# Optimization experiments

Hardware: AMD Instinct MI355X
Metric: run time of the kernel (lower is better)

Reference implementation:

```python
import jax, jax.numpy as jnp
import numpy as np

# SoftmaxMatMulSparse forward: out = softmax(x1, dim=-1) @ x2.
# The masker/sparsify/quantize path only compresses activations saved for
# backward; the forward output is the exact dense softmax-matmul.

def setup_inputs() -> dict:
    key = jax.random.key(0)
    k1, k2 = jax.random.split(key)
    x1 = jax.random.normal(k1, (1, 16, 2048, 2048), dtype=jnp.float32)  # [B,H,S,S] scores
    x2 = jax.random.normal(k2, (1, 16, 2048, 64), dtype=jnp.float32)    # [B,H,S,Dh] values
    return {"x1": x1, "x2": x2}

def reference(x1, x2):
    probs = jax.nn.softmax(x1, axis=-1)          # [B,H,S,S]
    return jnp.matmul(probs, x2)                 # [B,H,S,Dh]
```

## Files before the change

### kernel.cpp

```cpp
#include <hip/hip_runtime.h>
#include <hip/hip_bf16.h>
#include <stdint.h>


#define H_  16
#define S_  2048
#define D_  64
#define KT  128
#define QT  64

typedef short bf16x8 __attribute__((ext_vector_type(8)));
typedef float f32x4  __attribute__((ext_vector_type(4)));

__device__ __forceinline__ uint16_t f2bf(float f) {
  uint32_t u = __builtin_bit_cast(uint32_t, f);
  u += 0x7fffu + ((u >> 16) & 1u);
  return (uint16_t)(u >> 16);
}

__global__ __launch_bounds__(256) void vtrans_kernel(const float* __restrict__ x2,
                                                     uint16_t* __restrict__ x2t) {
  __shared__ float t[D_][64 + 1];
  const int h  = blockIdx.x >> 5;
  const int k0 = (blockIdx.x & 31) << 6;
  const float* src = x2 + ((size_t)h * S_ + k0) * D_;
#pragma unroll
  for (int p = 0; p < 4; ++p) {
    int flat = p * 1024 + threadIdx.x * 4;
    int k = flat >> 6, d = flat & 63;
    float4 v = *(const float4*)(src + (size_t)k * D_ + d);
    t[d + 0][k] = v.x; t[d + 1][k] = v.y; t[d + 2][k] = v.z; t[d + 3][k] = v.w;
  }
  __syncthreads();
  uint16_t* dst = x2t + (size_t)h * D_ * S_ + k0;
#pragma unroll
  for (int p = 0; p < 4; ++p) {
    int flat = p * 1024 + threadIdx.x * 4;
    int d = flat >> 6, k = flat & 63;
    ushort4 o;
    o.x = f2bf(t[d][k + 0]); o.y = f2bf(t[d][k + 1]);
    o.z = f2bf(t[d][k + 2]); o.w = f2bf(t[d][k + 3]);
    *(ushort4*)(dst + (size_t)d * S_ + k) = o;
  }
}

__global__ __launch_bounds__(256) void smm_kernel(const float* __restrict__ x1,
                                                  const float* __restrict__ x2,
                                                  const uint16_t* __restrict__ x2t,
                                                  int use_t,
                                                  float* __restrict__ out) {
  __shared__ __attribute__((aligned(16))) uint16_t pT[QT][KT];
  __shared__ __attribute__((aligned(16))) uint16_t vT[D_][KT];

  const int tid  = threadIdx.x;
  const int lane = tid & 63;
  const int w    = tid >> 6;
  const int h    = blockIdx.x >> 5;
  const int q0   = (blockIdx.x & 31) * QT;

  f32x4 acc[4];
  f32x4 accS;
#pragma unroll
  for (int c = 0; c < 4; ++c) acc[c] = (f32x4){0.f, 0.f, 0.f, 0.f};
  accS = (f32x4){0.f, 0.f, 0.f, 0.f};

  bf16x8 ones;
  {
    short v = ((lane & 15) == 0) ? (short)0x3F80 : (short)0;
#pragma unroll
    for (int e = 0; e < 8; ++e) ones[e] = v;
  }

  const float* x1p = x1 + ((size_t)h * S_ + q0) * S_;
  const int prow = tid >> 5;
  const int pk4  = (tid & 31) << 2;
  const int arow = lane & 15;
  const int kgrp = lane >> 4;

  for (int kt = 0; kt < S_ / KT; ++kt) {
    __syncthreads();

#pragma unroll
    for (int p = 0; p < 8; ++p) {
      int r = prow + p * 8;
      float4 v = *(const float4*)(x1p + (size_t)r * S_ + kt * KT + pk4);
      uint32_t lo = (uint32_t)f2bf(__expf(v.x)) | ((uint32_t)f2bf(__expf(v.y)) << 16);
      uint32_t hi = (uint32_t)f2bf(__expf(v.z)) | ((uint32_t)f2bf(__expf(v.w)) << 16);
      int byteoff = (pk4 * 2) ^ ((r & 15) << 4);
      *(uint2*)((char*)(&pT[r][0]) + byteoff) = make_uint2(lo, hi);
    }

    if (use_t) {
      const uint16_t* vp = x2t + (size_t)h * D_ * S_ + kt * KT;
#pragma unroll
      for (int p = 0; p < 4; ++p) {
        int flat = p * 256 + tid;
        int dd = flat >> 4;
        int ch = flat & 15;
        uint4 v = *(const uint4*)(vp + (size_t)dd * S_ + ch * 8);
        int byteoff = (ch * 16) ^ ((dd & 15) << 4);
        *(uint4*)((char*)(&vT[dd][0]) + byteoff) = v;
      }
    } else {
      int dd = tid & 63;
      int kg = tid >> 6;
      const float* src = x2 + ((size_t)h * S_ + kt * KT) * D_ + dd;
#pragma unroll
      for (int p = 0; p < 4; ++p) {
        int kb = p * 32 + kg * 8;
        uint16_t tmp[8];
#pragma unroll
        for (int j = 0; j < 8; ++j) tmp[j] = f2bf(src[(size_t)(kb + j) * D_]);
        int byteoff = (kb * 2) ^ ((dd & 15) << 4);
        *(uint4*)((char*)(&vT[dd][0]) + byteoff) = *(uint4*)tmp;
      }
    }
    __syncthreads();

#pragma unroll
    for (int ks = 0; ks < 4; ++ks) {
      int kb = ks * 64 + kgrp * 16;
      int ar = w * 16 + arow;
      bf16x8 a = *(const bf16x8*)((const char*)(&pT[ar][0]) + (kb ^ (arow << 4)));
      accS = __builtin_amdgcn_mfma_f32_16x16x32_bf16(a, ones, accS, 0, 0, 0);
#pragma unroll
      for (int c = 0; c < 4; ++c) {
        int bc = c * 16 + arow;
        bf16x8 b = *(const bf16x8*)((const char*)(&vT[bc][0]) + (kb ^ (arow << 4)));
        acc[c] = __builtin_amdgcn_mfma_f32_16x16x32_bf16(a, b, acc[c], 0, 0, 0);
      }
    }
  }

  float* op = out + ((size_t)h * S_ + q0 + w * 16) * D_;
#pragma unroll
  for (int j = 0; j < 4; ++j) {
    float s = __shfl(accS[j], lane & 48);
    float rs = 1.0f / s;
    int row = (lane >> 4) * 4 + j;
#pragma unroll
    for (int c = 0; c < 4; ++c) {
      op[(size_t)row * D_ + c * 16 + (lane & 15)] = acc[c][j] * rs;
    }
  }
}

extern "C" void kernel_launch(void* const* d_in, const int* in_sizes, int n_in,
                              void* d_out, int out_size, void* d_ws, size_t ws_size,
                              hipStream_t stream) {
  const float* x1 = (const float*)d_in[0];
  const float* x2 = (const float*)d_in[1];
  float* out      = (float*)d_out;
  uint16_t* x2t   = (uint16_t*)d_ws;

  const size_t need = (size_t)H_ * D_ * S_ * sizeof(uint16_t);
  int use_t = (ws_size >= need) ? 1 : 0;

  if (use_t) {
    vtrans_kernel<<<dim3(H_ * (S_ / 64)), dim3(256), 0, stream>>>(x2, x2t);
  }
  smm_kernel<<<dim3(H_ * (S_ / QT)), dim3(256), 0, stream>>>(x1, x2, x2t, use_t, out);
}
```

Measured before the change: 64.36 us.

## Use 128-row query tiles with 512 threads and swizzled block order

When the workspace is large enough, the main kernel now handles 128 query rows per block with 8 waves instead of 64 rows with 4 waves. Each staged V tile is then reused across twice as many rows, which halves the V load traffic per output row. Block IDs are remapped so that consecutive blocks go to different heads, likely to spread memory traffic. This halves the grid to 256 blocks, so occupancy and load balance across CUs may suffer.

```diff
diff --git a/kernel.cpp b/kernel.cpp
--- a/kernel.cpp
+++ b/kernel.cpp
@@ -6,8 +6,10 @@
 #define H_  16
 #define S_  2048
 #define D_  64
+#define QT  128
+#define QTF 64
 #define KT  128
-#define QT  64
+#define NT  (S_ / KT)
 
 typedef short bf16x8 __attribute__((ext_vector_type(8)));
 typedef float f32x4  __attribute__((ext_vector_type(4)));
@@ -44,19 +46,18 @@
   }
 }
 
-__global__ __launch_bounds__(256) void smm_kernel(const float* __restrict__ x1,
-                                                  const float* __restrict__ x2,
-                                                  const uint16_t* __restrict__ x2t,
-                                                  int use_t,
-                                                  float* __restrict__ out) {
+__global__ __launch_bounds__(512) void smm_q128(const float* __restrict__ x1,
+                                                const uint16_t* __restrict__ x2t,
+                                                float* __restrict__ out) {
   __shared__ __attribute__((aligned(16))) uint16_t pT[QT][KT];
   __shared__ __attribute__((aligned(16))) uint16_t vT[D_][KT];
 
+  const int bid  = ((int)blockIdx.x & 7) * 32 + ((int)blockIdx.x >> 3);
   const int tid  = threadIdx.x;
   const int lane = tid & 63;
   const int w    = tid >> 6;
-  const int h    = blockIdx.x >> 5;
-  const int q0   = (blockIdx.x & 31) * QT;
+  const int h    = bid >> 4;
+  const int q0   = (bid & 15) * QT;
 
   f32x4 acc[4];
   f32x4 accS;
@@ -77,9 +78,94 @@
   const int arow = lane & 15;
   const int kgrp = lane >> 4;
 
-  for (int kt = 0; kt < S_ / KT; ++kt) {
-    __syncthreads();
-
+  for (int kt = 0; kt < NT; ++kt) {
+    __syncthreads();
+
+#pragma unroll
+    for (int p = 0; p < 8; ++p) {
+      int r = prow + p * 16;
+      float4 v = *(const float4*)(x1p + (size_t)r * S_ + kt * KT + pk4);
+      uint32_t lo = (uint32_t)f2bf(__expf(v.x)) | ((uint32_t)f2bf(__expf(v.y)) << 16);
+      uint32_t hi = (uint32_t)f2bf(__expf(v.z)) | ((uint32_t)f2bf(__expf(v.w)) << 16);
+      int byteoff = (pk4 * 2) ^ ((r & 15) << 4);
+      *(uint2*)((char*)(&pT[r][0]) + byteoff) = make_uint2(lo, hi);
+    }
+
+    {
+      const uint16_t* vp = x2t + (size_t)h * D_ * S_ + kt * KT;
+#pragma unroll
+      for (int p = 0; p < 2; ++p) {
+        int flat = p * 512 + tid;
+        int dd = flat >> 4;
+        int ch = flat & 15;
+        uint4 v = *(const uint4*)(vp + (size_t)dd * S_ + ch * 8);
+        int byteoff = (ch * 16) ^ ((dd & 15) << 4);
+        *(uint4*)((char*)(&vT[dd][0]) + byteoff) = v;
+      }
+    }
+    __syncthreads();
+
+#pragma unroll
+    for (int ks = 0; ks < 4; ++ks) {
+      int kb = ks * 64 + kgrp * 16;
+      int ar = w * 16 + arow;
+      bf16x8 a = *(const bf16x8*)((const char*)(&pT[ar][0]) + (kb ^ (arow << 4)));
+      accS = __builtin_amdgcn_mfma_f32_16x16x32_bf16(a, ones, accS, 0, 0, 0);
+#pragma unroll
+      for (int c = 0; c < 4; ++c) {
+        int bc = c * 16 + arow;
+        bf16x8 b = *(const bf16x8*)((const char*)(&vT[bc][0]) + (kb ^ (arow << 4)));
+        acc[c] = __builtin_amdgcn_mfma_f32_16x16x32_bf16(a, b, acc[c], 0, 0, 0);
+      }
+    }
+  }
+
+  float* op = out + ((size_t)h * S_ + q0 + w * 16) * D_;
+#pragma unroll
+  for (int j = 0; j < 4; ++j) {
+    float s = __shfl(accS[j], lane & 48);
+    float rs = 1.0f / s;
+    int row = (lane >> 4) * 4 + j;
+#pragma unroll
+    for (int c = 0; c < 4; ++c) {
+      op[(size_t)row * D_ + c * 16 + (lane & 15)] = acc[c][j] * rs;
+    }
+  }
+}
+
+__global__ __launch_bounds__(256) void smm_lds(const float* __restrict__ x1,
+                                               const float* __restrict__ x2,
+                                               float* __restrict__ out) {
+  __shared__ __attribute__((aligned(16))) uint16_t pT[QTF][KT];
+  __shared__ __attribute__((aligned(16))) uint16_t vT[D_][KT];
+
+  const int tid  = threadIdx.x;
+  const int lane = tid & 63;
+  const int w    = tid >> 6;
+  const int h    = blockIdx.x >> 5;
+  const int q0   = (blockIdx.x & 31) * QTF;
+
+  f32x4 acc[4];
+  f32x4 accS;
+#pragma unroll
+  for (int c = 0; c < 4; ++c) acc[c] = (f32x4){0.f, 0.f, 0.f, 0.f};
+  accS = (f32x4){0.f, 0.f, 0.f, 0.f};
+
+  bf16x8 ones;
+  {
+    short v = ((lane & 15) == 0) ? (short)0x3F80 : (short)0;
+#pragma unroll
+    for (int e = 0; e < 8; ++e) ones[e] = v;
+  }
+
+  const float* x1p = x1 + ((size_t)h * S_ + q0) * S_;
+  const int prow = tid >> 5;
+  const int pk4  = (tid & 31) << 2;
+  const int arow = lane & 15;
+  const int kgrp = lane >> 4;
+
+  for (int kt = 0; kt < NT; ++kt) {
+    __syncthreads();
 #pragma unroll
     for (int p = 0; p < 8; ++p) {
       int r = prow + p * 8;
@@ -89,25 +175,13 @@
       int byteoff = (pk4 * 2) ^ ((r & 15) << 4);
       *(uint2*)((char*)(&pT[r][0]) + byteoff) = make_uint2(lo, hi);
     }
-
-    if (use_t) {
-      const uint16_t* vp = x2t + (size_t)h * D_ * S_ + kt * KT;
+    {
+      int dd = tid & 63;
+      int kgq = tid >> 6;
+      const float* src = x2 + ((size_t)h * S_ + kt * KT) * D_ + dd;
 #pragma unroll
       for (int p = 0; p < 4; ++p) {
-        int flat = p * 256 + tid;
-        int dd = flat >> 4;
-        int ch = flat & 15;
-        uint4 v = *(const uint4*)(vp + (size_t)dd * S_ + ch * 8);
-        int byteoff = (ch * 16) ^ ((dd & 15) << 4);
-        *(uint4*)((char*)(&vT[dd][0]) + byteoff) = v;
-      }
-    } else {
-      int dd = tid & 63;
-      int kg = tid >> 6;
-      const float* src = x2 + ((size_t)h * S_ + kt * KT) * D_ + dd;
-#pragma unroll
-      for (int p = 0; p < 4; ++p) {
-        int kb = p * 32 + kg * 8;
+        int kb = p * 32 + kgq * 8;
         uint16_t tmp[8];
 #pragma unroll
         for (int j = 0; j < 8; ++j) tmp[j] = f2bf(src[(size_t)(kb + j) * D_]);
@@ -116,7 +190,6 @@
       }
     }
     __syncthreads();
-
 #pragma unroll
     for (int ks = 0; ks < 4; ++ks) {
       int kb = ks * 64 + kgrp * 16;
@@ -154,10 +227,10 @@
   uint16_t* x2t   = (uint16_t*)d_ws;
 
   const size_t need = (size_t)H_ * D_ * S_ * sizeof(uint16_t);
-  int use_t = (ws_size >= need) ? 1 : 0;
-
-  if (use_t) {
+  if (ws_size >= need) {
     vtrans_kernel<<<dim3(H_ * (S_ / 64)), dim3(256), 0, stream>>>(x2, x2t);
-  }
-  smm_kernel<<<dim3(H_ * (S_ / QT)), dim3(256), 0, stream>>>(x1, x2, x2t, use_t, out);
-}
+    smm_q128<<<dim3(H_ * (S_ / QT)), dim3(512), 0, stream>>>(x1, x2t, out);
+  } else {
+    smm_lds<<<dim3(H_ * (S_ / QTF)), dim3(256), 0, stream>>>(x1, x2, out);
+  }
+}
```

Result: slower. 75.84 us (+17.8%).
